# Kernel tuning notes

Hardware: AMD Instinct MI355X
Metric: run time of the kernel (lower is better)

Reference implementation:

```python
import jax, jax.numpy as jnp
import numpy as np

B, S, D = 4, 2048, 1024


def setup_inputs() -> dict:
    key = jax.random.key(0)
    k1, k2, k3 = jax.random.split(key, 3)
    x = jax.random.normal(k1, (B, S, D), dtype=jnp.float32)
    # torch nn.Linear weights are [out_features, in_features]
    wq_w = jax.random.normal(k2, (D, D), dtype=jnp.float32) * (1.0 / np.sqrt(D))
    wv_w = jax.random.normal(k3, (D, D), dtype=jnp.float32) * (1.0 / np.sqrt(D))
    return {"x": x, "wq_w": wq_w, "wv_w": wv_w}


def reference(x, wq_w, wv_w):
    b, s, d = x.shape
    q = x @ wq_w.T                      # [B,S,D]
    kv = x @ wv_w.T                     # [B,S,D]  (original uses wv for BOTH k and v; wk unused)
    # original: k.view(B, k_dim, -1) -- a raw memory RESHAPE, not a transpose
    k_r = kv.reshape(b, d, s)           # [B,D,S]
    scores = jnp.einsum('bsd,bdt->bst', q, k_r) / np.sqrt(d)  # [B,S,S]
    sm = jax.nn.softmax(scores, axis=-1)
    sm = jnp.tril(sm)                   # post-softmax causal mask (rows NOT renormalized)
    return jnp.einsum('bst,btd->bsd', sm, kv)
```

## Files before the change

### kernel.cpp

```cpp
#include <hip/hip_runtime.h>


typedef __attribute__((ext_vector_type(8))) _Float16 f16x8;
typedef __attribute__((ext_vector_type(4))) _Float16 f16x4;
typedef __attribute__((ext_vector_type(4))) float f32x4;

__device__ __forceinline__ void glds16(const void* g, void* l) {
  __builtin_amdgcn_global_load_lds((const __attribute__((address_space(1))) void*)g,
                                   (__attribute__((address_space(3))) void*)l, 16, 0, 0);
}
#define BAR() __builtin_amdgcn_s_barrier()
#define LGKM0() do { asm volatile("s_waitcnt lgkmcnt(0)" ::: "memory"); \
                     __builtin_amdgcn_sched_barrier(0); } while (0)
#define VM2() asm volatile("s_waitcnt vmcnt(2)" ::: "memory")
#define VM0() asm volatile("s_waitcnt vmcnt(0)" ::: "memory")
#define VMLG0() asm volatile("s_waitcnt vmcnt(0) lgkmcnt(0)" ::: "memory")
#define PR1() __builtin_amdgcn_s_setprio(1)
#define PR0() __builtin_amdgcn_s_setprio(0)

__device__ __forceinline__ unsigned pkh2(float a, float b) {
  union { _Float16 h[2]; unsigned u; } c;
  c.h[0] = (_Float16)a; c.h[1] = (_Float16)b;
  return c.u;
}

__global__ __launch_bounds__(256) void cvt3(const float* __restrict__ x,
                                            const float* __restrict__ wq,
                                            const float* __restrict__ wv,
                                            _Float16* __restrict__ xh,
                                            _Float16* __restrict__ wqh,
                                            _Float16* __restrict__ wvh) {
  int i = blockIdx.x * 256 + threadIdx.x;
  const float* src;
  _Float16* dst;
  int off;
  if (i < 2097152) { src = x; dst = xh; off = i; }
  else if (i < 2359296) { src = wq; dst = wqh; off = i - 2097152; }
  else { src = wv; dst = wvh; off = i - 2359296; }
  float4 v = ((const float4*)src)[off];
  f16x4 o = {(_Float16)v.x, (_Float16)v.y, (_Float16)v.z, (_Float16)v.w};
  ((f16x4*)dst)[off] = o;
}

template <typename OUT_T, int EPI>
__global__ __launch_bounds__(512, 2) void gemm8p(const _Float16* __restrict__ A,
                                                 const _Float16* __restrict__ BT,
                                                 OUT_T* __restrict__ C,
                                                 _Float16* __restrict__ T1,
                                                 _Float16* __restrict__ T2,
                                                 int K, int ldc,
                                                 long sA, long sB, long sC, float scale,
                                                 int lgx, int lgy) {
  extern __shared__ char smem[];
  _Float16* lds = (_Float16*)smem;
  const int lin = blockIdx.x + gridDim.x * (blockIdx.y + gridDim.y * blockIdx.z);
  const int xcd = lin & 7, s = lin >> 3;
  int mx, ny, bz;
  if (EPI == 1) {
    mx = (xcd << 2) | (s >> 3);
    const int nyz = s & 7;
    ny = nyz & 3;
    bz = nyz >> 2;
  } else {
    const int G = (gridDim.y * gridDim.z) >> 3;
    mx = s & ((1 << lgx) - 1);
    const int pid = xcd * G + (s >> lgx);
    ny = pid & (gridDim.y - 1);
    bz = pid >> lgy;
  }
  A += (size_t)bz * sA;
  BT += (size_t)bz * sB;
  C += (size_t)bz * sC;
  const int m0 = mx << 8, n0 = ny << 8;
  const int tid = threadIdx.x, lane = tid & 63, wave = tid >> 6;
  const int wm = wave >> 2, wn = wave & 3;
  const int lr = lane & 15, lk = lane >> 4, xr = lane & 7;
  const int nkt = K >> 6;
  const int A0 = 0, A1 = 8192, B0 = 16384, B1 = 24576, BUF = 32768;
  const int baseA = wm ? A1 : A0;
  const int baseB = B0 + ((wn >> 1) << 13);
  const int bRow = (wn & 1) << 6;
  const int srow = lane >> 3;
  const int scolB = ((lane & 7) << 4) ^ (srow << 4);

  f32x4 acc[8][4] = {};
  f16x8 fa[4][2], fb[4][2];

#define STAGE(bufsel, halfsel, G_, hrow0, kt) do {                                   \
    const _Float16* _g = (G_) + (size_t)((hrow0) + wave * 16 + srow) * K + ((kt) << 6); \
    glds16((const char*)_g + scolB, (char*)&lds[(bufsel) * BUF + (halfsel) + wave * 1024]); \
    glds16((const char*)(_g + (size_t)8 * K) + scolB,                                \
           (char*)&lds[(bufsel) * BUF + (halfsel) + wave * 1024 + 512]);             \
  } while (0)
#define RDA(buf, mf, ks) (*(const f16x8*)&lds[(buf) * BUF + baseA + ((mf) * 16 + lr) * 64 + \
                                              ((((ks) * 4 + lk) ^ xr) << 3)])
#define RDB(buf, nf, ks) (*(const f16x8*)&lds[(buf) * BUF + baseB + (bRow + (nf) * 16 + lr) * 64 + \
                                              ((((ks) * 4 + lk) ^ xr) << 3)])
#define RDFA4(b, mbase) do { _Pragma("unroll")                                        \
    for (int i = 0; i < 4; ++i) { fa[i][0] = RDA(b, (mbase) + i, 0);                  \
                                  fa[i][1] = RDA(b, (mbase) + i, 1); } } while (0)
#define RDFB2(b, jbase) do { _Pragma("unroll")                                        \
    for (int j = 0; j < 2; ++j) { fb[(jbase) + j][0] = RDB(b, (jbase) + j, 0);        \
                                  fb[(jbase) + j][1] = RDB(b, (jbase) + j, 1); } } while (0)
#define MMQ(ib, jb) do { _Pragma("unroll")                                            \
    for (int i = 0; i < 4; ++i) { _Pragma("unroll")                                   \
      for (int j = 0; j < 2; ++j) {                                                   \
        acc[(ib) + i][(jb) + j] = __builtin_amdgcn_mfma_f32_16x16x32_f16(             \
            fa[i][0], fb[(jb) + j][0], acc[(ib) + i][(jb) + j], 0, 0, 0);             \
        acc[(ib) + i][(jb) + j] = __builtin_amdgcn_mfma_f32_16x16x32_f16(             \
            fa[i][1], fb[(jb) + j][1], acc[(ib) + i][(jb) + j], 0, 0, 0);             \
      } } } while (0)

  STAGE(0, A0, A, m0, 0);
  STAGE(0, A1, A, m0 + 128, 0);
  STAGE(0, B0, BT, n0, 0);
  STAGE(0, B1, BT, n0 + 128, 0);
  STAGE(1, A0, A, m0, 1);
  VM2();
  BAR();

  for (int it = 0; it < (nkt >> 1); ++it) {
    const int t = it << 1;
    const int t2 = (t + 2 < nkt) ? t + 2 : 0;
    const int t3 = (t + 3 < nkt) ? t + 3 : 0;
    RDFA4(0, 0); RDFB2(0, 0); RDFB2(0, 2);
    STAGE(1, A1, A, m0 + 128, t + 1);
    STAGE(1, B0, BT, n0, t + 1);
    STAGE(1, B1, BT, n0 + 128, t + 1);
    BAR(); LGKM0(); PR1(); MMQ(0, 0); MMQ(0, 2); PR0(); BAR();
    RDFA4(0, 4);
    STAGE(0, A0, A, m0, t2);
    VM2();
    BAR(); LGKM0(); PR1(); MMQ(4, 2); MMQ(4, 0); PR0(); BAR();
    RDFA4(1, 0); RDFB2(1, 0); RDFB2(1, 2);
    STAGE(0, A1, A, m0 + 128, t2);
    STAGE(0, B0, BT, n0, t2);
    STAGE(0, B1, BT, n0 + 128, t2);
    BAR(); LGKM0(); PR1(); MMQ(0, 0); MMQ(0, 2); PR0(); BAR();
    RDFA4(1, 4);
    STAGE(1, A0, A, m0, t3);
    VM2();
    BAR(); LGKM0(); PR1(); MMQ(4, 2); MMQ(4, 0); PR0(); BAR();
  }

  if (EPI == 1 && bz == 1) {
    const int b = m0 >> 11;
    _Float16* kvvT = T1 + ((size_t)b << 21);
    _Float16* kvT  = T2 + ((size_t)b << 21);
    const int tb = (m0 & 2047) + wm * 128;
    const int db = n0 + wn * 64;
    char* wlds = smem + wave * 16384;
#pragma unroll
    for (int mf = 0; mf < 8; ++mf)
#pragma unroll
      for (int nf = 0; nf < 4; ++nf) {
        const int tl = mf * 16 + lk * 4;
        const int dl = nf * 16 + lr;
        const f32x4 a = acc[mf][nf];
        uint2 w = {pkh2(a[0], a[1]), pkh2(a[2], a[3])};
        *(uint2*)(wlds + dl * 256 + ((tl * 2) ^ ((dl & 7) << 4))) = w;
      }
#pragma unroll
    for (int it2 = 0; it2 < 32; ++it2) {
      const int dl = it2 * 2 + (lane >> 5);
      const int d = db + dl;
      const int tseg = (lane & 31) * 4;
      uint2 v = *(const uint2*)(wlds + dl * 256 + ((tseg * 2) ^ ((dl & 7) << 4)));
      *(uint2*)(kvT + (size_t)d * 2048 + tb + tseg) = v;
      unsigned ev = (v.x & 0xFFFFu) | (v.y << 16);
      unsigned od = (v.x >> 16) | (v.y & 0xFFFF0000u);
      const int k0 = (tb + tseg) >> 1;
      *(unsigned*)(kvvT + (size_t)d * 1024 + k0) = ev;
      *(unsigned*)(kvvT + (size_t)(1024 + d) * 1024 + k0) = od;
    }
  } else if (EPI == 2) {
    float* Pst = (float*)T1 + (size_t)bz * 2048 * 32;
    const int gidx = ny * 4 + wn;
    const bool wr = (n0 <= m0);
#pragma unroll
    for (int mf = 0; mf < 8; ++mf) {
      float e[4][4];
#pragma unroll
      for (int nf = 0; nf < 4; ++nf)
#pragma unroll
        for (int r = 0; r < 4; ++r)
          e[nf][r] = __expf(acc[mf][nf][r] * scale - 8.0f);
      const int row = m0 + wm * 128 + mf * 16 + lk * 4;
#pragma unroll
      for (int r = 0; r < 4; ++r) {
        float sm = (e[0][r] + e[1][r]) + (e[2][r] + e[3][r]);
#pragma unroll
        for (int off = 1; off < 16; off <<= 1) sm += __shfl_xor(sm, off);
        if (lr == 0) Pst[(size_t)(row + r) * 32 + gidx] = sm;
      }
      if (wr) {
#pragma unroll
        for (int nf = 0; nf < 4; ++nf) {
          const int col = n0 + wn * 64 + nf * 16 + lr;
#pragma unroll
          for (int r = 0; r < 4; ++r)
            C[(size_t)(row + r) * ldc + col] =
                (OUT_T)((col <= row + r) ? e[nf][r] : 0.f);
        }
      }
    }
  } else {
#pragma unroll
    for (int mf = 0; mf < 8; ++mf)
#pragma unroll
      for (int nf = 0; nf < 4; ++nf) {
        const int row = m0 + wm * 128 + mf * 16 + lk * 4;
        const int col = n0 + wn * 64 + nf * 16 + lr;
#pragma unroll
        for (int r = 0; r < 4; ++r)
          C[(size_t)(row + r) * ldc + col] = (OUT_T)(acc[mf][nf][r] * scale);
      }
  }
#undef STAGE
#undef RDA
#undef RDB
#undef RDFA4
#undef RDFB2
#undef MMQ
}

__global__ __launch_bounds__(256) void gemm_pv_bal(const _Float16* __restrict__ P,
                                                   const _Float16* __restrict__ KVT,
                                                   const float* __restrict__ Pst,
                                                   float* __restrict__ Out,
                                                   long sA, long sB, long sC) {
  __shared__ _Float16 As[2][64 * 64];
  __shared__ _Float16 Bs[2][128 * 64];
  __shared__ float StL[2][64];
  const int total = gridDim.x * gridDim.y * gridDim.z;
  int lin = blockIdx.x + gridDim.x * (blockIdx.y + gridDim.y * blockIdx.z);
  const int xcd = lin & 7, slot = lin >> 3;
  const int perx = total >> 7;
  const int grp = xcd * perx + (slot >> 4);
  const int p = slot & 15;
  const int ny = grp & 7, bz = grp >> 3;
  P += (size_t)bz * sA;
  KVT += (size_t)bz * sB;
  Out += (size_t)bz * sC;
  Pst += (size_t)bz * 2048 * 32;
  const int n0 = ny * 128;
  const int tid = threadIdx.x;
  const int lane = tid & 63, wave = tid >> 6;
  const int fr = lane & 15, lk = lane >> 4;
  const int srow = lane >> 3;
  const int scol = (((lane & 7) ^ srow) << 4);

#define PSTAGE(buf, m0s, t) do {                                                     \
    const int _k0 = (t) << 6;                                                        \
    _Pragma("unroll")                                                                \
    for (int c = 0; c < 2; ++c) {                                                    \
      const int ch = wave * 2 + c;                                                   \
      glds16((const char*)(P + (size_t)((m0s) + ch * 8 + srow) * 2048 + _k0) + scol, \
             &As[buf][ch * 512]);                                                    \
    }                                                                                \
    _Pragma("unroll")                                                                \
    for (int c = 0; c < 4; ++c) {                                                    \
      const int ch = wave * 4 + c;                                                   \
      glds16((const char*)(KVT + (size_t)(n0 + ch * 8 + srow) * 2048 + _k0) + scol,  \
             &Bs[buf][ch * 512]);                                                    \
    }                                                                                \
  } while (0)

#pragma unroll
  for (int half = 0; half < 2; ++half) {
    const int strip = half ? (31 - p) : p;
    const int m0s = strip * 64;
    const int nt = strip + 1;
    if (tid < 64) {
      const float4* pp = (const float4*)(Pst + (size_t)(m0s + tid) * 32);
      float l = 0.f;
#pragma unroll
      for (int g = 0; g < 8; ++g) {
        float4 v = pp[g];
        l += (v.x + v.y) + (v.z + v.w);
      }
      StL[half][tid] = 1.f / l;
    }
    f32x4 acc[4][2] = {};
    PSTAGE(0, m0s, 0);
    VMLG0();
    BAR();
    for (int t = 0; t < nt; ++t) {
      const int cur = t & 1;
      if (t + 1 < nt) PSTAGE(cur ^ 1, m0s, t + 1);
      f16x8 af[4][2], bf[2][2];
#pragma unroll
      for (int m = 0; m < 4; ++m) {
        const int r = m * 16 + fr;
#pragma unroll
        for (int ks = 0; ks < 2; ++ks)
          af[m][ks] = *(const f16x8*)&As[cur][r * 64 + (((ks * 4 + lk) ^ (r & 7)) << 3)];
      }
#pragma unroll
      for (int n = 0; n < 2; ++n) {
        const int rb = wave * 32 + n * 16 + fr;
#pragma unroll
        for (int ks = 0; ks < 2; ++ks)
          bf[n][ks] = *(const f16x8*)&Bs[cur][rb * 64 + (((ks * 4 + lk) ^ (rb & 7)) << 3)];
      }
      LGKM0();
      PR1();
#pragma unroll
      for (int ks = 0; ks < 2; ++ks)
#pragma unroll
        for (int m = 0; m < 4; ++m)
#pragma unroll
          for (int n = 0; n < 2; ++n)
            acc[m][n] = __builtin_amdgcn_mfma_f32_16x16x32_f16(af[m][ks], bf[n][ks],
                                                               acc[m][n], 0, 0, 0);
      PR0();
      VM0();
      BAR();
    }
#pragma unroll
    for (int m = 0; m < 4; ++m) {
      const int rl = m * 16 + lk * 4;
      const int row = m0s + rl;
      float cr[4];
#pragma unroll
      for (int r = 0; r < 4; ++r) cr[r] = StL[half][rl + r];
#pragma unroll
      for (int n = 0; n < 2; ++n) {
        const int col = n0 + wave * 32 + n * 16 + fr;
#pragma unroll
        for (int r = 0; r < 4; ++r)
          Out[(size_t)(row + r) * 1024 + col] = acc[m][n][r] * cr[r];
      }
    }
  }
#undef PSTAGE
}

extern "C" void kernel_launch(void* const* d_in, const int* in_sizes, int n_in,
                              void* d_out, int out_size, void* d_ws, size_t ws_size,
                              hipStream_t stream) {
  const float* x = (const float*)d_in[0];
  const float* wq = (const float*)d_in[1];
  const float* wv = (const float*)d_in[2];
  float* out = (float*)d_out;
  char* ws = (char*)d_ws;

  const size_t MB = 1024 * 1024;
  const int bc = (ws_size >= 88 * MB) ? 4 : 2;
  const size_t scBytes = (size_t)bc * 2048 * 2048 * 2;
  const long PB = 2048 * 1024;
  const long SB = (long)2048 * 2048;

  _Float16* Sc = (_Float16*)ws;
  _Float16* qh = (_Float16*)(ws + scBytes);
  _Float16* kvvT = (_Float16*)(ws + scBytes + 16 * MB);
  _Float16* kvT = (_Float16*)(ws + scBytes + 32 * MB);
  _Float16* wqh = (_Float16*)(ws + scBytes + 48 * MB);
  _Float16* wvh = (_Float16*)(ws + scBytes + 50 * MB);
  float* Pst = (float*)(ws + scBytes + 52 * MB);
  _Float16* xh = (_Float16*)ws;

  cvt3<<<10240, 256, 0, stream>>>(x, wq, wv, xh, wqh, wvh);

  gemm8p<_Float16, 1><<<dim3(32, 4, 2), 512, 131072, stream>>>(
      xh, wqh, qh, kvvT, kvT, 1024, 1024, 0, (long)(wvh - wqh), 0, 1.0f, 5, 2);

  for (int b0 = 0; b0 < 4; b0 += bc) {
    gemm8p<_Float16, 2><<<dim3(8, 8, bc), 512, 131072, stream>>>(
        qh + (size_t)b0 * PB, kvvT + (size_t)b0 * PB, Sc, (_Float16*)Pst, nullptr,
        1024, 2048, PB, PB, SB, 0.03125f, 3, 3);
    gemm_pv_bal<<<dim3(16, 8, bc), 256, 0, stream>>>(
        Sc, kvT + (size_t)b0 * PB, Pst, out + (size_t)b0 * PB, SB, PB, PB);
  }
}
```

Measured before the change: 121.8 us.

## Replace 256x256 pipelined GEMM with simpler 128x128 double-buffered GEMM

```diff
diff --git a/kernel.cpp b/kernel.cpp
--- a/kernel.cpp
+++ b/kernel.cpp
@@ -12,7 +12,6 @@
 #define BAR() __builtin_amdgcn_s_barrier()
 #define LGKM0() do { asm volatile("s_waitcnt lgkmcnt(0)" ::: "memory"); \
                      __builtin_amdgcn_sched_barrier(0); } while (0)
-#define VM2() asm volatile("s_waitcnt vmcnt(2)" ::: "memory")
 #define VM0() asm volatile("s_waitcnt vmcnt(0)" ::: "memory")
 #define VMLG0() asm volatile("s_waitcnt vmcnt(0) lgkmcnt(0)" ::: "memory")
 #define PR1() __builtin_amdgcn_s_setprio(1)
@@ -43,24 +42,24 @@
 }
 
 template <typename OUT_T, int EPI>
-__global__ __launch_bounds__(512, 2) void gemm8p(const _Float16* __restrict__ A,
-                                                 const _Float16* __restrict__ BT,
-                                                 OUT_T* __restrict__ C,
-                                                 _Float16* __restrict__ T1,
-                                                 _Float16* __restrict__ T2,
-                                                 int K, int ldc,
-                                                 long sA, long sB, long sC, float scale,
-                                                 int lgx, int lgy) {
-  extern __shared__ char smem[];
-  _Float16* lds = (_Float16*)smem;
+__global__ __launch_bounds__(512, 4) void gemm128(const _Float16* __restrict__ A,
+                                                  const _Float16* __restrict__ BT,
+                                                  OUT_T* __restrict__ C,
+                                                  _Float16* __restrict__ T1,
+                                                  _Float16* __restrict__ T2,
+                                                  int K, int ldc,
+                                                  long sA, long sB, long sC, float scale,
+                                                  int lgx, int lgy) {
+  __shared__ _Float16 As[2][128 * 64];
+  __shared__ _Float16 Bs[2][128 * 64];
   const int lin = blockIdx.x + gridDim.x * (blockIdx.y + gridDim.y * blockIdx.z);
   const int xcd = lin & 7, s = lin >> 3;
   int mx, ny, bz;
   if (EPI == 1) {
-    mx = (xcd << 2) | (s >> 3);
-    const int nyz = s & 7;
-    ny = nyz & 3;
-    bz = nyz >> 2;
+    mx = (xcd << 3) | (s >> 4);
+    const int nyz = s & 15;
+    ny = nyz & 7;
+    bz = nyz >> 3;
   } else {
     const int G = (gridDim.y * gridDim.z) >> 3;
     mx = s & ((1 << lgx) - 1);
@@ -71,101 +70,87 @@
   A += (size_t)bz * sA;
   BT += (size_t)bz * sB;
   C += (size_t)bz * sC;
-  const int m0 = mx << 8, n0 = ny << 8;
+  const int m0 = mx << 7, n0 = ny << 7;
   const int tid = threadIdx.x, lane = tid & 63, wave = tid >> 6;
   const int wm = wave >> 2, wn = wave & 3;
-  const int lr = lane & 15, lk = lane >> 4, xr = lane & 7;
-  const int nkt = K >> 6;
-  const int A0 = 0, A1 = 8192, B0 = 16384, B1 = 24576, BUF = 32768;
-  const int baseA = wm ? A1 : A0;
-  const int baseB = B0 + ((wn >> 1) << 13);
-  const int bRow = (wn & 1) << 6;
+  const int fr = lane & 15, lk = lane >> 4;
   const int srow = lane >> 3;
-  const int scolB = ((lane & 7) << 4) ^ (srow << 4);
-
-  f32x4 acc[8][4] = {};
-  f16x8 fa[4][2], fb[4][2];
-
-#define STAGE(bufsel, halfsel, G_, hrow0, kt) do {                                   \
-    const _Float16* _g = (G_) + (size_t)((hrow0) + wave * 16 + srow) * K + ((kt) << 6); \
-    glds16((const char*)_g + scolB, (char*)&lds[(bufsel) * BUF + (halfsel) + wave * 1024]); \
-    glds16((const char*)(_g + (size_t)8 * K) + scolB,                                \
-           (char*)&lds[(bufsel) * BUF + (halfsel) + wave * 1024 + 512]);             \
+  const int scol = (((lane & 7) ^ srow) << 4);
+  const int nt = K >> 6;
+
+  f32x4 acc[4][2] = {};
+
+#define GSTAGE(buf, t) do {                                                          \
+    const int _k0 = (t) << 6;                                                        \
+    _Pragma("unroll")                                                                \
+    for (int c = 0; c < 2; ++c) {                                                    \
+      const int ch = wave * 2 + c;                                                   \
+      glds16((const char*)(A + (size_t)(m0 + ch * 8 + srow) * K + _k0) + scol,       \
+             &As[buf][ch * 512]);                                                    \
+      glds16((const char*)(BT + (size_t)(n0 + ch * 8 + srow) * K + _k0) + scol,      \
+             &Bs[buf][ch * 512]);                                                    \
+    }                                                                                \
   } while (0)
-#define RDA(buf, mf, ks) (*(const f16x8*)&lds[(buf) * BUF + baseA + ((mf) * 16 + lr) * 64 + \
-                                              ((((ks) * 4 + lk) ^ xr) << 3)])
-#define RDB(buf, nf, ks) (*(const f16x8*)&lds[(buf) * BUF + baseB + (bRow + (nf) * 16 + lr) * 64 + \
-                                              ((((ks) * 4 + lk) ^ xr) << 3)])
-#define RDFA4(b, mbase) do { _Pragma("unroll")                                        \
-    for (int i = 0; i < 4; ++i) { fa[i][0] = RDA(b, (mbase) + i, 0);                  \
-                                  fa[i][1] = RDA(b, (mbase) + i, 1); } } while (0)
-#define RDFB2(b, jbase) do { _Pragma("unroll")                                        \
-    for (int j = 0; j < 2; ++j) { fb[(jbase) + j][0] = RDB(b, (jbase) + j, 0);        \
-                                  fb[(jbase) + j][1] = RDB(b, (jbase) + j, 1); } } while (0)
-#define MMQ(ib, jb) do { _Pragma("unroll")                                            \
-    for (int i = 0; i < 4; ++i) { _Pragma("unroll")                                   \
-      for (int j = 0; j < 2; ++j) {                                                   \
-        acc[(ib) + i][(jb) + j] = __builtin_amdgcn_mfma_f32_16x16x32_f16(             \
-            fa[i][0], fb[(jb) + j][0], acc[(ib) + i][(jb) + j], 0, 0, 0);             \
-        acc[(ib) + i][(jb) + j] = __builtin_amdgcn_mfma_f32_16x16x32_f16(             \
-            fa[i][1], fb[(jb) + j][1], acc[(ib) + i][(jb) + j], 0, 0, 0);             \
-      } } } while (0)
-
-  STAGE(0, A0, A, m0, 0);
-  STAGE(0, A1, A, m0 + 128, 0);
-  STAGE(0, B0, BT, n0, 0);
-  STAGE(0, B1, BT, n0 + 128, 0);
-  STAGE(1, A0, A, m0, 1);
-  VM2();
+
+  GSTAGE(0, 0);
+  VM0();
   BAR();
-
-  for (int it = 0; it < (nkt >> 1); ++it) {
-    const int t = it << 1;
-    const int t2 = (t + 2 < nkt) ? t + 2 : 0;
-    const int t3 = (t + 3 < nkt) ? t + 3 : 0;
-    RDFA4(0, 0); RDFB2(0, 0); RDFB2(0, 2);
-    STAGE(1, A1, A, m0 + 128, t + 1);
-    STAGE(1, B0, BT, n0, t + 1);
-    STAGE(1, B1, BT, n0 + 128, t + 1);
-    BAR(); LGKM0(); PR1(); MMQ(0, 0); MMQ(0, 2); PR0(); BAR();
-    RDFA4(0, 4);
-    STAGE(0, A0, A, m0, t2);
-    VM2();
-    BAR(); LGKM0(); PR1(); MMQ(4, 2); MMQ(4, 0); PR0(); BAR();
-    RDFA4(1, 0); RDFB2(1, 0); RDFB2(1, 2);
-    STAGE(0, A1, A, m0 + 128, t2);
-    STAGE(0, B0, BT, n0, t2);
-    STAGE(0, B1, BT, n0 + 128, t2);
-    BAR(); LGKM0(); PR1(); MMQ(0, 0); MMQ(0, 2); PR0(); BAR();
-    RDFA4(1, 4);
-    STAGE(1, A0, A, m0, t3);
-    VM2();
-    BAR(); LGKM0(); PR1(); MMQ(4, 2); MMQ(4, 0); PR0(); BAR();
+  for (int t = 0; t < nt; ++t) {
+    const int cur = t & 1;
+    if (t + 1 < nt) GSTAGE(cur ^ 1, t + 1);
+    f16x8 af[4][2], bf[2][2];
+#pragma unroll
+    for (int m = 0; m < 4; ++m) {
+      const int r = wm * 64 + m * 16 + fr;
+#pragma unroll
+      for (int ks = 0; ks < 2; ++ks)
+        af[m][ks] = *(const f16x8*)&As[cur][r * 64 + (((ks * 4 + lk) ^ (r & 7)) << 3)];
+    }
+#pragma unroll
+    for (int n = 0; n < 2; ++n) {
+      const int rb = wn * 32 + n * 16 + fr;
+#pragma unroll
+      for (int ks = 0; ks < 2; ++ks)
+        bf[n][ks] = *(const f16x8*)&Bs[cur][rb * 64 + (((ks * 4 + lk) ^ (rb & 7)) << 3)];
+    }
+    LGKM0();
+    PR1();
+#pragma unroll
+    for (int ks = 0; ks < 2; ++ks)
+#pragma unroll
+      for (int m = 0; m < 4; ++m)
+#pragma unroll
+        for (int n = 0; n < 2; ++n)
+          acc[m][n] = __builtin_amdgcn_mfma_f32_16x16x32_f16(af[m][ks], bf[n][ks],
+                                                             acc[m][n], 0, 0, 0);
+    PR0();
+    VM0();
+    BAR();
   }
 
   if (EPI == 1 && bz == 1) {
     const int b = m0 >> 11;
     _Float16* kvvT = T1 + ((size_t)b << 21);
     _Float16* kvT  = T2 + ((size_t)b << 21);
-    const int tb = (m0 & 2047) + wm * 128;
-    const int db = n0 + wn * 64;
-    char* wlds = smem + wave * 16384;
-#pragma unroll
-    for (int mf = 0; mf < 8; ++mf)
-#pragma unroll
-      for (int nf = 0; nf < 4; ++nf) {
+    const int tb = (m0 & 2047) + wm * 64;
+    const int db = n0 + wn * 32;
+    char* wlds = (char*)&As[0][0] + wave * 4096;
+#pragma unroll
+    for (int mf = 0; mf < 4; ++mf)
+#pragma unroll
+      for (int nf = 0; nf < 2; ++nf) {
         const int tl = mf * 16 + lk * 4;
-        const int dl = nf * 16 + lr;
+        const int dl = nf * 16 + fr;
         const f32x4 a = acc[mf][nf];
         uint2 w = {pkh2(a[0], a[1]), pkh2(a[2], a[3])};
-        *(uint2*)(wlds + dl * 256 + ((tl * 2) ^ ((dl & 7) << 4))) = w;
-      }
-#pragma unroll
-    for (int it2 = 0; it2 < 32; ++it2) {
-      const int dl = it2 * 2 + (lane >> 5);
+        *(uint2*)(wlds + dl * 128 + ((tl * 2) ^ ((dl & 7) << 4))) = w;
+      }
+#pragma unroll
+    for (int it2 = 0; it2 < 8; ++it2) {
+      const int dl = it2 * 4 + (lane >> 4);
       const int d = db + dl;
-      const int tseg = (lane & 31) * 4;
-      uint2 v = *(const uint2*)(wlds + dl * 256 + ((tseg * 2) ^ ((dl & 7) << 4)));
+      const int tseg = (lane & 15) * 4;
+      uint2 v = *(const uint2*)(wlds + dl * 128 + ((tseg * 2) ^ ((dl & 7) << 4)));
       *(uint2*)(kvT + (size_t)d * 2048 + tb + tseg) = v;
       unsigned ev = (v.x & 0xFFFFu) | (v.y << 16);
       unsigned od = (v.x >> 16) | (v.y & 0xFFFF0000u);
@@ -174,29 +159,29 @@
       *(unsigned*)(kvvT + (size_t)(1024 + d) * 1024 + k0) = od;
     }
   } else if (EPI == 2) {
-    float* Pst = (float*)T1 + (size_t)bz * 2048 * 32;
-    const int gidx = ny * 4 + wn;
+    float* Pst = (float*)T1 + (size_t)bz * 2048 * 64;
+    const int gidx = (n0 >> 5) + wn;
     const bool wr = (n0 <= m0);
 #pragma unroll
-    for (int mf = 0; mf < 8; ++mf) {
-      float e[4][4];
-#pragma unroll
-      for (int nf = 0; nf < 4; ++nf)
+    for (int mf = 0; mf < 4; ++mf) {
+      float e[2][4];
+#pragma unroll
+      for (int nf = 0; nf < 2; ++nf)
 #pragma unroll
         for (int r = 0; r < 4; ++r)
           e[nf][r] = __expf(acc[mf][nf][r] * scale - 8.0f);
-      const int row = m0 + wm * 128 + mf * 16 + lk * 4;
+      const int row = m0 + wm * 64 + mf * 16 + lk * 4;
 #pragma unroll
       for (int r = 0; r < 4; ++r) {
-        float sm = (e[0][r] + e[1][r]) + (e[2][r] + e[3][r]);
+        float sm = e[0][r] + e[1][r];
 #pragma unroll
         for (int off = 1; off < 16; off <<= 1) sm += __shfl_xor(sm, off);
-        if (lr == 0) Pst[(size_t)(row + r) * 32 + gidx] = sm;
+        if (fr == 0) Pst[(size_t)(row + r) * 64 + gidx] = sm;
       }
       if (wr) {
 #pragma unroll
-        for (int nf = 0; nf < 4; ++nf) {
-          const int col = n0 + wn * 64 + nf * 16 + lr;
+        for (int nf = 0; nf < 2; ++nf) {
+          const int col = n0 + wn * 32 + nf * 16 + fr;
 #pragma unroll
           for (int r = 0; r < 4; ++r)
             C[(size_t)(row + r) * ldc + col] =
@@ -206,22 +191,17 @@
     }
   } else {
 #pragma unroll
-    for (int mf = 0; mf < 8; ++mf)
-#pragma unroll
-      for (int nf = 0; nf < 4; ++nf) {
-        const int row = m0 + wm * 128 + mf * 16 + lk * 4;
-        const int col = n0 + wn * 64 + nf * 16 + lr;
+    for (int mf = 0; mf < 4; ++mf)
+#pragma unroll
+      for (int nf = 0; nf < 2; ++nf) {
+        const int row = m0 + wm * 64 + mf * 16 + lk * 4;
+        const int col = n0 + wn * 32 + nf * 16 + fr;
 #pragma unroll
         for (int r = 0; r < 4; ++r)
           C[(size_t)(row + r) * ldc + col] = (OUT_T)(acc[mf][nf][r] * scale);
       }
   }
-#undef STAGE
-#undef RDA
-#undef RDB
-#undef RDFA4
-#undef RDFB2
-#undef MMQ
+#undef GSTAGE
 }
 
 __global__ __launch_bounds__(256) void gemm_pv_bal(const _Float16* __restrict__ P,
@@ -242,7 +222,7 @@
   P += (size_t)bz * sA;
   KVT += (size_t)bz * sB;
   Out += (size_t)bz * sC;
-  Pst += (size_t)bz * 2048 * 32;
+  Pst += (size_t)bz * 2048 * 64;
   const int n0 = ny * 128;
   const int tid = threadIdx.x;
   const int lane = tid & 63, wave = tid >> 6;
@@ -272,10 +252,10 @@
     const int m0s = strip * 64;
     const int nt = strip + 1;
     if (tid < 64) {
-      const float4* pp = (const float4*)(Pst + (size_t)(m0s + tid) * 32);
+      const float4* pp = (const float4*)(Pst + (size_t)(m0s + tid) * 64);
       float l = 0.f;
 #pragma unroll
-      for (int g = 0; g < 8; ++g) {
+      for (int g = 0; g < 16; ++g) {
         float4 v = pp[g];
         l += (v.x + v.y) + (v.z + v.w);
       }
@@ -362,13 +342,13 @@
 
   cvt3<<<10240, 256, 0, stream>>>(x, wq, wv, xh, wqh, wvh);
 
-  gemm8p<_Float16, 1><<<dim3(32, 4, 2), 512, 131072, stream>>>(
-      xh, wqh, qh, kvvT, kvT, 1024, 1024, 0, (long)(wvh - wqh), 0, 1.0f, 5, 2);
+  gemm128<_Float16, 1><<<dim3(64, 8, 2), 512, 0, stream>>>(
+      xh, wqh, qh, kvvT, kvT, 1024, 1024, 0, (long)(wvh - wqh), 0, 1.0f, 0, 0);
 
   for (int b0 = 0; b0 < 4; b0 += bc) {
-    gemm8p<_Float16, 2><<<dim3(8, 8, bc), 512, 131072, stream>>>(
+    gemm128<_Float16, 2><<<dim3(16, 16, bc), 512, 0, stream>>>(
         qh + (size_t)b0 * PB, kvvT + (size_t)b0 * PB, Sc, (_Float16*)Pst, nullptr,
-        1024, 2048, PB, PB, SB, 0.03125f, 3, 3);
+        1024, 2048, PB, PB, SB, 0.03125f, 4, 4);
     gemm_pv_bal<<<dim3(16, 8, bc), 256, 0, stream>>>(
         Sc, kvT + (size_t)b0 * PB, Pst, out + (size_t)b0 * PB, SB, PB, PB);
   }
```

New measurement: 133.8 us. 1.1x slower.
